# Performance work log

Measured on AMD Instinct MI355X. Metric: run time of the kernel, lower is better.

## Reference

```python
import jax, jax.numpy as jnp
import numpy as np
from jax import lax

D = 128      # d_model
NH = 8       # nhead
DIM = D // NH
B, H, W = 2, 160, 160
EPS_ATT = 1e-6


def setup_inputs() -> dict:
    key = jax.random.key(0)
    ks = iter(jax.random.split(key, 40))
    def n(*s):
        return jax.random.normal(next(ks), s, dtype=jnp.float32) * 0.05
    inp = {
        "x": jax.random.normal(next(ks), (B, D, H, W), jnp.float32),
        "source": jax.random.normal(next(ks), (B, D, H, W), jnp.float32),
        # q/k/v 1x1 conv (with bias)
        "wq": n(D, D), "bq": n(D),
        "wk": n(D, D), "bk": n(D),
        "wv": n(D, D), "bv": n(D),
        # multiscale aggregation (scale=5): depthwise 5x5 (no bias) + pointwise 1x1 (no bias)
        "dwq": n(D, 1, 5, 5), "pwq": n(D, D),
        "dwk": n(D, 1, 5, 5), "pwk": n(D, D),
        "dwv": n(D, 1, 5, 5), "pwv": n(D, D),
        # attention output projection: 2*d_model -> d_model, no bias
        "wproj": n(D, 2 * D),
        # merge 1x1 conv
        "wmerge": n(D, D), "bmerge": n(D),
        # conv ffn: d -> 2d -> d
        "wff1": n(2 * D, D), "bff1": n(2 * D),
        "wff2": n(D, 2 * D), "bff2": n(D),
        # layernorms over channel dim
        "ln1_w": 1.0 + n(D), "ln1_b": n(D),
        "ln2_w": 1.0 + n(D), "ln2_b": n(D),
    }
    return inp


def _pw(t, Wm, b=None):
    # 1x1 conv as channel matmul; t: [B,C,H,W], Wm: [O,C]
    y = jnp.einsum('bchw,oc->bohw', t, Wm)
    return y if b is None else y + b[None, :, None, None]


def _bn(t):
    # BatchNorm2d, training-mode batch stats, affine=False, eps=1e-5
    m = t.mean((0, 2, 3), keepdims=True)
    v = t.var((0, 2, 3), keepdims=True)
    return (t - m) * lax.rsqrt(v + 1e-5)


def _gelu(t):
    return jax.nn.gelu(t, approximate=False)


def _dw(t, Wk):
    # depthwise 5x5 conv, stride 1, SAME padding (== padding=2)
    return lax.conv_general_dilated(t, Wk, (1, 1), 'SAME',
                                    dimension_numbers=('NCHW', 'OIHW', 'NCHW'),
                                    feature_group_count=D)


def _ln(t, w, b):
    # LayerNorm over channel axis of NCHW tensor, eps=1e-5
    m = t.mean(1, keepdims=True)
    v = t.var(1, keepdims=True)
    return (t - m) * lax.rsqrt(v + 1e-5) * w[None, :, None, None] + b[None, :, None, None]


def reference(x, source, wq, bq, wk, bk, wv, bv, dwq, pwq, dwk, pwk, dwv, pwv,
              wproj, wmerge, bmerge, wff1, bff1, wff2, bff2,
              ln1_w, ln1_b, ln2_w, ln2_b):
    q = _gelu(_bn(_pw(x, wq, bq)))
    k = _gelu(_bn(_pw(source, wk, bk)))
    v = _gelu(_bn(_pw(source, wv, bv)))

    # multiscale aggregation: concat original with one scale-5 depthwise+pointwise branch
    qc = jnp.concatenate([q, _pw(_dw(q, dwq), pwq)], axis=1)
    kc = jnp.concatenate([k, _pw(_dw(k, dwk), pwk)], axis=1)
    vc = jnp.concatenate([v, _pw(_dw(v, dwv), pwv)], axis=1)

    qc = jax.nn.relu(qc)  # kernel feature map
    kc = jax.nn.relu(kc)

    b_, C2, h1, w1 = qc.shape           # C2 = 2*d_model
    h2, w2 = kc.shape[2], kc.shape[3]
    L1, L2 = h1 * w1, h2 * w2
    H2 = C2 // DIM                       # effective heads = 2*nhead

    qf = qc.reshape(b_, C2, L1).transpose(0, 2, 1).reshape(b_, L1, H2, DIM)
    kf = kc.reshape(b_, C2, L2).transpose(0, 2, 1).reshape(b_, L2, H2, DIM)
    vf = vc.reshape(b_, C2, L2).transpose(0, 2, 1).reshape(b_, L2, H2, DIM)

    vf = vf / L2
    kv = jnp.einsum('nshd,nshv->nhdv', kf, vf)                       # [b,H2,d,d]
    z = 1.0 / jnp.maximum(jnp.einsum('nlhd,nhd->nlh', qf, kf.sum(1) / L2), EPS_ATT)
    qv = jnp.einsum('nlhd,nhdv,nlh->nlhv', qf, kv, z)                # [b,L1,H2,d]

    out = qv.transpose(0, 2, 3, 1).reshape(b_, C2, h1, w1)
    msg = _pw(out, wproj)                                            # 2d -> d

    msg = _gelu(_bn(_pw(msg, wmerge, bmerge)))
    msg = x + msg
    msg = _ln(msg, ln1_w, ln1_b)

    ff = _gelu(_bn(_pw(msg, wff1, bff1)))
    ff = _gelu(_bn(_pw(ff, wff2, bff2)))
    return _ln(ff + msg, ln2_w, ln2_b)
```

## Files before the change

### kernel.cpp

```cpp
#include <hip/hip_runtime.h>
#include <math.h>

#define LL 25600
#define NTOTF 51200.f
#define NSH 8

using f16   = _Float16;
using f16x8 = __attribute__((ext_vector_type(8))) _Float16;
using f16x4 = __attribute__((ext_vector_type(4))) _Float16;
using f16x2 = __attribute__((ext_vector_type(2))) _Float16;
using f32x4 = __attribute__((ext_vector_type(4))) float;

__device__ __forceinline__ float gelu_f(float v) {
    const float u2 = v * (1.5957691216057308f + 0.0713548162726009f * v * v);
    const float e  = __expf(u2);
    return v * (1.f - 1.f / (e + 1.f));
}

__device__ __forceinline__ void stat_mr(const float* st, int C, int c,
                                        float& m, float& r) {
    float s1 = 0.f, s2 = 0.f;
#pragma unroll
    for (int sh = 0; sh < NSH; ++sh) {
        s1 += st[sh * 2 * C + c];
        s2 += st[sh * 2 * C + C + c];
    }
    m = s1 * (1.f / NTOTF);
    r = rsqrtf(s2 * (1.f / NTOTF) - m * m + 1e-5f);
}

template <int M, int K, int PP, int NSEG, bool IN32, bool LDG, bool TWOW,
          bool BIAS, bool STATS>
__global__ __launch_bounds__(512, 2) void gemm_kernel(
    const void* __restrict__ X1, const void* __restrict__ X2,
    const void* __restrict__ X3,
    const float* __restrict__ WA, const float* __restrict__ WB,
    const float* __restrict__ W2, const float* __restrict__ W3,
    const float* __restrict__ biasA, const float* __restrict__ biasB,
    const float* __restrict__ lstat,
    f16* __restrict__ Y1, f16* __restrict__ Y2, f16* __restrict__ Y3,
    float* __restrict__ ostat)
{
    constexpr int MR  = M / 128;
    constexpr int KS  = K / 32;
    constexpr int NR  = PP / 16;
    constexpr int PG  = PP / 8;
    constexpr int NCH = (K * PG) / 512;
    constexpr int NCHUNK = LL / PP;

    __shared__ f16 Xs[PP * K];

    const int tid  = threadIdx.x;
    const int lane = tid & 63;
    const int wv   = tid >> 6;
    const int lm16 = lane & 15, lg = lane >> 4;
    const int row0 = wv * (M / 8);

    int bx = blockIdx.x, seg = 0;
    if (NSEG > 1) { seg = bx / (2 * NCHUNK); bx -= seg * 2 * NCHUNK; }
    const int bb  = bx / NCHUNK;
    const int pp0 = (bx - bb * NCHUNK) * PP;

    const void*  Xp = (NSEG > 1) ? (seg == 0 ? X1 : (seg == 1 ? X2 : X3)) : X1;
    const float* Wp = (NSEG > 1) ? (seg == 0 ? WA : (seg == 1 ? W2 : W3)) : WA;
    f16*         Yp = (NSEG > 1) ? (seg == 0 ? Y1 : (seg == 1 ? Y2 : Y3)) : Y1;

    const int c0  = (tid / PG) * NCH;
    const int p0g = (tid % PG) * 8;

    f16x8 xin[NCH];
#pragma unroll
    for (int cc = 0; cc < NCH; ++cc) {
        const size_t roff = (size_t)(bb * K + c0 + cc) * LL + pp0 + p0g;
        if (IN32) {
            const float4 a  = *reinterpret_cast<const float4*>(
                                  reinterpret_cast<const float*>(Xp) + roff);
            const float4 b2 = *reinterpret_cast<const float4*>(
                                  reinterpret_cast<const float*>(Xp) + roff + 4);
            f16x8 v;
            v[0] = (f16)a.x;  v[1] = (f16)a.y;  v[2] = (f16)a.z;  v[3] = (f16)a.w;
            v[4] = (f16)b2.x; v[5] = (f16)b2.y; v[6] = (f16)b2.z; v[7] = (f16)b2.w;
            xin[cc] = v;
        } else {
            xin[cc] = *reinterpret_cast<const f16x8*>(
                          reinterpret_cast<const f16*>(Xp) + roff);
        }
    }

    f16x8 wfr[KS][MR];
#pragma unroll
    for (int k = 0; k < KS; ++k) {
        const int col = k * 32 + lg * 8;
#pragma unroll
        for (int mr = 0; mr < MR; ++mr) {
            const int row = row0 + mr * 16 + lm16;
            const float* wp = (TWOW && row >= 128)
                                  ? WB + (size_t)(row - 128) * K + col
                                  : Wp + (size_t)row * K + col;
            const float4 wa = *reinterpret_cast<const float4*>(wp);
            const float4 wb2 = *reinterpret_cast<const float4*>(wp + 4);
            f16x8 v;
            v[0] = (f16)wa.x; v[1] = (f16)wa.y; v[2] = (f16)wa.z; v[3] = (f16)wa.w;
            v[4] = (f16)wb2.x; v[5] = (f16)wb2.y; v[6] = (f16)wb2.z; v[7] = (f16)wb2.w;
            wfr[k][mr] = v;
        }
    }

    float bvv[MR], st1[MR], st2[MR];
#pragma unroll
    for (int mr = 0; mr < MR; ++mr) {
        const int o = row0 + mr * 16 + lm16;
        bvv[mr] = BIAS ? ((TWOW && o >= 128) ? biasB[o - 128] : biasA[o]) : 0.f;
        st1[mr] = 0.f; st2[mr] = 0.f;
    }

    if (LDG) {
#pragma unroll
        for (int cc = 0; cc < NCH; ++cc) {
            const int c = c0 + cc;
            float m, r;
            stat_mr(lstat, K, c, m, r);
#pragma unroll
            for (int j = 0; j < 8; ++j)
                xin[cc][j] = (f16)gelu_f(((float)xin[cc][j] - m) * r);
        }
    }

#pragma unroll
    for (int j = 0; j < 8; ++j) {
        const int pos = p0g + j;
        const int swz = ((pos & 7) ^ ((pos >> 3) & 7)) << 3;
        if constexpr (NCH == 8) {
            f16x8 v;
#pragma unroll
            for (int cc = 0; cc < 8; ++cc) v[cc] = xin[cc][j];
            *reinterpret_cast<f16x8*>(&Xs[(size_t)pos * K + (c0 ^ swz)]) = v;
        } else if constexpr (NCH == 4) {
            f16x4 v;
#pragma unroll
            for (int cc = 0; cc < 4; ++cc) v[cc] = xin[cc][j];
            *reinterpret_cast<f16x4*>(&Xs[(size_t)pos * K + (c0 ^ swz)]) = v;
        } else {
            f16x2 v;
#pragma unroll
            for (int cc = 0; cc < 2; ++cc) v[cc] = xin[cc][j];
            *reinterpret_cast<f16x2*>(&Xs[(size_t)pos * K + (c0 ^ swz)]) = v;
        }
    }
    __syncthreads();

    f32x4 acc[MR][NR];
#pragma unroll
    for (int mr = 0; mr < MR; ++mr)
#pragma unroll
        for (int nr = 0; nr < NR; ++nr)
            acc[mr][nr] = (f32x4){0.f, 0.f, 0.f, 0.f};

#pragma unroll
    for (int k = 0; k < KS; ++k) {
        const int kc = k * 32 + lg * 8;
        f16x8 xa[NR];
#pragma unroll
        for (int nr = 0; nr < NR; ++nr) {
            const int pos = nr * 16 + lm16;
            const int swz = ((pos & 7) ^ ((pos >> 3) & 7)) << 3;
            xa[nr] = *reinterpret_cast<const f16x8*>(
                &Xs[(size_t)pos * K + (kc ^ swz)]);
        }
#pragma unroll
        for (int mr = 0; mr < MR; ++mr)
#pragma unroll
            for (int nr = 0; nr < NR; ++nr)
                acc[mr][nr] = __builtin_amdgcn_mfma_f32_16x16x32_f16(
                    xa[nr], wfr[k][mr], acc[mr][nr], 0, 0, 0);
    }

#pragma unroll
    for (int mr = 0; mr < MR; ++mr) {
        const int o = row0 + mr * 16 + lm16;
        f16* yb = Yp + (size_t)(bb * M + o) * LL + pp0;
#pragma unroll
        for (int nr = 0; nr < NR; ++nr) {
            f16x4 o4;
#pragma unroll
            for (int r = 0; r < 4; ++r) {
                const float v = acc[mr][nr][r] + bvv[mr];
                o4[r] = (f16)v;
                if (STATS) { st1[mr] += v; st2[mr] += v * v; }
            }
            *reinterpret_cast<f16x4*>(yb + nr * 16 + lg * 4) = o4;
        }
    }

    if (STATS) {
        float* osb = ostat + (size_t)(blockIdx.x & (NSH - 1)) * 2 * M;
#pragma unroll
        for (int mr = 0; mr < MR; ++mr) {
            float s1 = st1[mr], s2 = st2[mr];
            s1 += __shfl_xor(s1, 16); s2 += __shfl_xor(s2, 16);
            s1 += __shfl_xor(s1, 32); s2 += __shfl_xor(s2, 32);
            if (lane < 16) {
                const int o = row0 + mr * 16 + lm16;
                atomicAdd(&osb[o], s1);
                atomicAdd(&osb[M + o], s2);
            }
        }
    }
}

__global__ __launch_bounds__(256) void act_kernel(
    const f16* __restrict__ qraw, const f16* __restrict__ kvraw,
    const float* __restrict__ sQ, const float* __restrict__ sKV,
    f16* __restrict__ actq, f16* __restrict__ actkv)
{
    const int idx = blockIdx.x * 256 + threadIdx.x;
    const f16* src; f16* dst; const float* st; int C, local;
    if (idx < 819200) { src = qraw;  dst = actq;  st = sQ;  C = 128; local = idx; }
    else              { src = kvraw; dst = actkv; st = sKV; C = 256; local = idx - 819200; }
    const int c = (local / 3200) % C;
    float m, r;
    stat_mr(st, C, c, m, r);
    const f16x8 v = *reinterpret_cast<const f16x8*>(src + (size_t)local * 8);
    f16x8 o;
#pragma unroll
    for (int j = 0; j < 8; ++j)
        o[j] = (f16)gelu_f(((float)v[j] - m) * r);
    *reinterpret_cast<f16x8*>(dst + (size_t)local * 8) = o;
}

__global__ __launch_bounds__(256) void dw5_kernel(
    const f16* __restrict__ actq, const f16* __restrict__ actkv,
    const float* __restrict__ dwq, const float* __restrict__ dwk,
    const float* __restrict__ dwv,
    f16* __restrict__ oq, f16* __restrict__ ok, f16* __restrict__ ov)
{
    __shared__ f16x2 pt[20][41];
    const int z = blockIdx.z;
    const int which = z >> 8;
    const int bc = z & 255;
    const int b = bc >> 7, c = bc & 127;

    const f16* src; const float* wdwp; f16* outp;
    if (which == 0)      { src = actq  + (size_t)(b * 128 + c) * LL;       wdwp = dwq + c * 25; outp = oq; }
    else if (which == 1) { src = actkv + (size_t)(b * 256 + c) * LL;       wdwp = dwk + c * 25; outp = ok; }
    else                 { src = actkv + (size_t)(b * 256 + 128 + c) * LL; wdwp = dwv + c * 25; outp = ov; }

    const int h0 = blockIdx.y * 32, w0 = blockIdx.x * 32;
    const int tid = threadIdx.x;

    f16x2 wp[25];
#pragma unroll
    for (int q = 0; q < 25; ++q) {
        const f16 wv16 = (f16)wdwp[q];
        wp[q][0] = wv16; wp[q][1] = wv16;
    }

    for (int idx = tid; idx < 720; idx += 256) {
        const int t  = idx / 36, cc = idx - t * 36;
        const int iw = w0 - 2 + cc;
        const int ih0 = h0 - 2 + t, ih1 = ih0 + 16;
        const int iwc  = min(max(iw, 0), 159);
        const int ihc0 = min(max(ih0, 0), 159);
        const int ihc1 = min(max(ih1, 0), 159);
        const bool okw = (iw >= 0) & (iw < 160);
        f16 lo = src[ihc0 * 160 + iwc];
        f16 hi = src[ihc1 * 160 + iwc];
        if (!(okw & (ih0 >= 0) & (ih0 < 160))) lo = (f16)0;
        if (!(okw & (ih1 >= 0) & (ih1 < 160))) hi = (f16)0;
        f16x2 pv; pv[0] = lo; pv[1] = hi;
        pt[t][cc] = pv;
    }
    __syncthreads();

    const int ylo = tid >> 4, xq = tid & 15, x0 = xq * 2;

    f16x2 a0; a0[0] = (f16)0; a0[1] = (f16)0;
    f16x2 a1 = a0;
#pragma unroll
    for (int u = 0; u < 5; ++u) {
        const f16x2* row = &pt[ylo + u][x0];
        const f16x2 r0 = row[0], r1 = row[1], r2 = row[2];
        const f16x2 r3 = row[3], r4 = row[4], r5 = row[5];
        a0 += wp[u*5+0] * r0;  a1 += wp[u*5+0] * r1;
        a0 += wp[u*5+1] * r1;  a1 += wp[u*5+1] * r2;
        a0 += wp[u*5+2] * r2;  a1 += wp[u*5+2] * r3;
        a0 += wp[u*5+3] * r3;  a1 += wp[u*5+3] * r4;
        a0 += wp[u*5+4] * r4;  a1 += wp[u*5+4] * r5;
    }

    f16* ob = outp + (size_t)(b * 128 + c) * LL + (size_t)(h0 + ylo) * 160 + (w0 + x0);
    f16x2 lo2; lo2[0] = a0[0]; lo2[1] = a1[0];
    f16x2 hi2; hi2[0] = a0[1]; hi2[1] = a1[1];
    *reinterpret_cast<f16x2*>(ob) = lo2;
    *reinterpret_cast<f16x2*>(ob + 16 * 160) = hi2;
}

__global__ __launch_bounds__(256) void att_reduce_kernel(
    const f16* __restrict__ ACT, const f16* __restrict__ K2,
    const f16* __restrict__ V2,
    float* __restrict__ kvout, float* __restrict__ ksum)
{
    __shared__ float kvred[4][256];

    const int bx = blockIdx.x;
    const int b = bx / 400;
    const int rem = bx - b * 400;
    const int h = rem / 25;
    const int chunk = rem - h * 25;
    const int tid = threadIdx.x;
    const int wv = tid >> 6, l = tid & 63;
    const int ch = l & 15, kg = l >> 4;
    const bool half1 = h < 8;

    const f16* kbase = half1 ? ACT + (size_t)(b * 256 + h * 16 + ch) * LL
                             : K2 + (size_t)(b * 128 + (h - 8) * 16 + ch) * LL;
    const f16* vbase = half1 ? ACT + (size_t)(b * 256 + 128 + h * 16 + ch) * LL
                             : V2 + (size_t)(b * 128 + (h - 8) * 16 + ch) * LL;

    f32x4 acc = (f32x4){0.f, 0.f, 0.f, 0.f};
    float ksacc = 0.f;
    const int base = chunk * 1024 + kg * 8;
#pragma unroll
    for (int it = 0; it < 8; ++it) {
        const int p = base + wv * 256 + it * 32;
        const f16x8 kf = *reinterpret_cast<const f16x8*>(kbase + p);
        const f16x8 vf = *reinterpret_cast<const f16x8*>(vbase + p);
        f16x8 ka;
#pragma unroll
        for (int j = 0; j < 8; ++j) {
            const f16 kv_ = kf[j];
            ka[j] = (kv_ > (f16)0) ? kv_ : (f16)0;
            ksacc += (float)ka[j];
        }
        acc = __builtin_amdgcn_mfma_f32_16x16x32_f16(ka, vf, acc, 0, 0, 0);
    }

    constexpr float s = 1.f / (float)LL;
#pragma unroll
    for (int r = 0; r < 4; ++r)
        kvred[wv][(kg * 4 + r) * 16 + ch] = acc[r];
    __syncthreads();
    {
        float t = kvred[0][tid] + kvred[1][tid] + kvred[2][tid] + kvred[3][tid];
        atomicAdd(&kvout[(size_t)(b * 16 + h) * 256 + tid], t * s);
    }

    float s1 = ksacc;
    s1 += __shfl_xor(s1, 16);
    s1 += __shfl_xor(s1, 32);
    if (l < 16) atomicAdd(&ksum[(size_t)(b * 16 + h) * 16 + ch], s1 * s);
}

__global__ __launch_bounds__(256) void att_apply_kernel(
    const f16* __restrict__ Q, const f16* __restrict__ Q2,
    const float* __restrict__ kvin, const float* __restrict__ ksumin,
    f16* __restrict__ att)
{
    __shared__ float kvs[256];
    __shared__ float kss[16];

    const int bx = blockIdx.x;
    const int b = bx / 1600;
    const int rem = bx - b * 1600;
    const int h = rem / 100;
    const int chunk = rem - h * 100;
    const int tid = threadIdx.x;
    const int p = chunk * 256 + tid;

    kvs[tid] = kvin[(size_t)b * 4096 + h * 256 + tid];
    if (tid < 16) kss[tid] = ksumin[(size_t)b * 256 + h * 16 + tid];
    __syncthreads();

    const f16* qb = (h < 8) ? Q + (size_t)(b * 128 + h * 16) * LL
                            : Q2 + (size_t)(b * 128 + (h - 8) * 16) * LL;
    float s[16];
#pragma unroll
    for (int d = 0; d < 16; ++d)
        s[d] = fmaxf((float)qb[(size_t)d * LL + p], 0.f);
    float denom = 0.f;
#pragma unroll
    for (int d = 0; d < 16; ++d) denom = fmaf(s[d], kss[d], denom);
    const float z = 1.f / fmaxf(denom, 1e-6f);

    f16* ob = att + (size_t)(b * 256 + h * 16) * LL + p;
#pragma unroll
    for (int e = 0; e < 16; ++e) {
        float acc = 0.f;
#pragma unroll
        for (int d = 0; d < 16; ++d)
            acc = fmaf(s[d], kvs[d * 16 + e], acc);
        ob[(size_t)e * LL] = (f16)(acc * z);
    }
}

template <bool RES32, bool OUT32>
__global__ __launch_bounds__(256) void fuse_ln_kernel(
    const f16* __restrict__ yconv, const void* __restrict__ residv,
    const float* __restrict__ stat,
    const float* __restrict__ lnw, const float* __restrict__ lnb,
    void* __restrict__ outv)
{
    __shared__ float t[128][64];
    __shared__ float mrs[128][2];
    __shared__ float red[4][64][2];
    __shared__ float mln[64], rln[64];

    const int bx = blockIdx.x;
    const int b = bx / 400, p0 = (bx - b * 400) * 64;
    const int tid = threadIdx.x;

    if (tid < 128) {
        float m, r;
        stat_mr(stat, 128, tid, m, r);
        mrs[tid][0] = m; mrs[tid][1] = r;
    }
    __syncthreads();

    for (int idx = tid; idx < 8192; idx += 256) {
        const int c = idx >> 6, i = idx & 63;
        const size_t off = (size_t)(b * 128 + c) * LL + p0 + i;
        const float g = gelu_f(((float)yconv[off] - mrs[c][0]) * mrs[c][1]);
        const float r = RES32 ? reinterpret_cast<const float*>(residv)[off]
                              : (float)reinterpret_cast<const f16*>(residv)[off];
        t[c][i] = g + r;
    }
    __syncthreads();

    {
        const int i = tid & 63, q = tid >> 6;
        float ps = 0.f, pq = 0.f;
        for (int c = q * 32; c < q * 32 + 32; ++c) {
            const float v = t[c][i];
            ps += v; pq += v * v;
        }
        red[q][i][0] = ps; red[q][i][1] = pq;
    }
    __syncthreads();
    if (tid < 64) {
        float s1 = 0.f, s2 = 0.f;
#pragma unroll
        for (int q = 0; q < 4; ++q) { s1 += red[q][tid][0]; s2 += red[q][tid][1]; }
        const float m = s1 * (1.f / 128.f);
        const float var = s2 * (1.f / 128.f) - m * m;
        mln[tid] = m; rln[tid] = rsqrtf(var + 1e-5f);
    }
    __syncthreads();

    for (int idx = tid; idx < 8192; idx += 256) {
        const int c = idx >> 6, i = idx & 63;
        const float v = (t[c][i] - mln[i]) * rln[i] * lnw[c] + lnb[c];
        const size_t off = (size_t)(b * 128 + c) * LL + p0 + i;
        if (OUT32) reinterpret_cast<float*>(outv)[off] = v;
        else reinterpret_cast<f16*>(outv)[off] = (f16)v;
    }
}

__global__ __launch_bounds__(256) void wcomb_kernel(
    const float* __restrict__ wmerge, const float* __restrict__ wproj,
    float* __restrict__ wc)
{
    const int o = blockIdx.x;
    const int c2 = threadIdx.x;
    float acc = 0.f;
#pragma unroll 4
    for (int m = 0; m < 128; ++m)
        acc = fmaf(wmerge[o * 128 + m], wproj[m * 256 + c2], acc);
    wc[o * 256 + c2] = acc;
}

extern "C" void kernel_launch(void* const* d_in, const int* in_sizes, int n_in,
                              void* d_out, int out_size, void* d_ws, size_t ws_size,
                              hipStream_t stream)
{
    const float* x      = (const float*)d_in[0];
    const float* source = (const float*)d_in[1];
    const float* wq = (const float*)d_in[2];  const float* bq = (const float*)d_in[3];
    const float* wk = (const float*)d_in[4];  const float* bk = (const float*)d_in[5];
    const float* wvw = (const float*)d_in[6]; const float* bvb = (const float*)d_in[7];
    const float* dwq = (const float*)d_in[8];  const float* pwq = (const float*)d_in[9];
    const float* dwk = (const float*)d_in[10]; const float* pwk = (const float*)d_in[11];
    const float* dwv = (const float*)d_in[12]; const float* pwv = (const float*)d_in[13];
    const float* wproj  = (const float*)d_in[14];
    const float* wmerge = (const float*)d_in[15]; const float* bmerge = (const float*)d_in[16];
    const float* wff1 = (const float*)d_in[17]; const float* bff1 = (const float*)d_in[18];
    const float* wff2 = (const float*)d_in[19]; const float* bff2 = (const float*)d_in[20];
    const float* ln1w = (const float*)d_in[21]; const float* ln1b = (const float*)d_in[22];
    const float* ln2w = (const float*)d_in[23]; const float* ln2b = (const float*)d_in[24];

    const size_t UNIT  = (size_t)2 * 128 * LL;
    const size_t UNITB = UNIT * sizeof(f16);
    char* w = (char*)d_ws;
    f16* qraw  = (f16*)w; w += UNITB;
    f16* kvraw = (f16*)w; w += 2 * UNITB;
    f16* actq  = (f16*)w; w += UNITB;
    f16* actkv = (f16*)w; w += 2 * UNITB;
    f16* q2raw = (f16*)w; w += UNITB;
    f16* k2raw = (f16*)w; w += UNITB;
    f16* v2raw = (f16*)w; w += UNITB;
    f16* y2raw = (f16*)w; w += UNITB;
    f16* msg   = (f16*)w; w += UNITB;
    f16* ff1raw= (f16*)w; w += 2 * UNITB;
    f16* ff2raw= (f16*)w; w += UNITB;

    f16* dtq = qraw;
    f16* dtk = kvraw;
    f16* dtv = kvraw + UNIT;
    f16* att = actkv;

    float* zbase = (float*)w;
    float* kvred = zbase;
    float* ksum  = zbase + 8192;
    float* sQ    = zbase + 8704;
    float* sKV   = sQ + NSH * 256;
    float* sM    = sKV + NSH * 512;
    float* sF1   = sM + NSH * 256;
    float* sF2   = sF1 + NSH * 512;
    const size_t zcount = 8192 + 512 + NSH * (256 + 512 + 256 + 512 + 256);
    float* wcomb = zbase + zcount;

    hipMemsetAsync(zbase, 0, zcount * sizeof(float), stream);
    wcomb_kernel<<<128, 256, 0, stream>>>(wmerge, wproj, wcomb);

    gemm_kernel<128,128,128,1,true,false,false,true,true><<<400, 512, 0, stream>>>(
        x, nullptr, nullptr, wq, nullptr, nullptr, nullptr, bq, nullptr, nullptr,
        qraw, nullptr, nullptr, sQ);
    gemm_kernel<256,128,64,1,true,false,true,true,true><<<800, 512, 0, stream>>>(
        source, nullptr, nullptr, wk, wvw, nullptr, nullptr, bk, bvb, nullptr,
        kvraw, nullptr, nullptr, sKV);

    act_kernel<<<9600, 256, 0, stream>>>(qraw, kvraw, sQ, sKV, actq, actkv);

    dim3 dwg(5, 5, 768);
    dw5_kernel<<<dwg, 256, 0, stream>>>(actq, actkv, dwq, dwk, dwv, dtq, dtk, dtv);
    gemm_kernel<128,128,128,3,false,false,false,false,false><<<1200, 512, 0, stream>>>(
        dtq, dtk, dtv, pwq, nullptr, pwk, pwv, nullptr, nullptr, nullptr,
        q2raw, k2raw, v2raw, nullptr);

    att_reduce_kernel<<<800, 256, 0, stream>>>(actkv, k2raw, v2raw, kvred, ksum);
    att_apply_kernel<<<3200, 256, 0, stream>>>(actq, q2raw, kvred, ksum, att);

    gemm_kernel<128,256,128,1,false,false,false,true,true><<<400, 512, 0, stream>>>(
        att, nullptr, nullptr, wcomb, nullptr, nullptr, nullptr, bmerge, nullptr,
        nullptr, y2raw, nullptr, nullptr, sM);

    fuse_ln_kernel<true,false><<<800, 256, 0, stream>>>(
        y2raw, x, sM, ln1w, ln1b, msg);

    gemm_kernel<256,128,64,1,false,false,false,true,true><<<800, 512, 0, stream>>>(
        msg, nullptr, nullptr, wff1, nullptr, nullptr, nullptr, bff1, nullptr,
        nullptr, ff1raw, nullptr, nullptr, sF1);
    gemm_kernel<128,256,128,1,false,true,false,true,true><<<400, 512, 0, stream>>>(
        ff1raw, nullptr, nullptr, wff2, nullptr, nullptr, nullptr, bff2, nullptr,
        sF1, ff2raw, nullptr, nullptr, sF2);

    fuse_ln_kernel<false,true><<<800, 256, 0, stream>>>(
        ff2raw, msg, sF2, ln2w, ln2b, (float*)d_out);
}
```

Before: 273.3 us.

## Fuse attention apply with merged projection GEMM into one kernel

Replaces the separate attention-apply kernel and the following 256->128 projection GEMM with a single kernel. Each block computes the linear-attention output for 64 pixels across all 16 heads into swizzled shared memory, then runs MFMA against the combined weight and accumulates BN statistics. This removes the write and re-read of the 256-channel fp16 attention tensor and one launch. In exchange, each block redundantly loads all kv matrices and converts weights, and it uses more shared memory per block.

```diff
diff --git a/kernel.cpp b/kernel.cpp
--- a/kernel.cpp
+++ b/kernel.cpp
@@ -208,6 +208,127 @@
     }
 }
 
+__global__ __launch_bounds__(512, 2) void att_merge_kernel(
+    const f16* __restrict__ Q, const f16* __restrict__ Q2,
+    const float* __restrict__ kvin, const float* __restrict__ ksumin,
+    const float* __restrict__ wc, const float* __restrict__ bias,
+    f16* __restrict__ Y, float* __restrict__ ostat)
+{
+    __shared__ f16 Xs[64 * 256];
+    __shared__ float kvs[4096];
+    __shared__ float kss[256];
+
+    const int tid  = threadIdx.x;
+    const int lane = tid & 63;
+    const int wv   = tid >> 6;
+    const int lm16 = lane & 15, lg = lane >> 4;
+    const int row0 = wv * 16;
+
+    const int bx = blockIdx.x;
+    const int b  = bx / 400;
+    const int p0 = (bx - b * 400) * 64;
+
+    for (int i = tid; i < 4096; i += 512) kvs[i] = kvin[(size_t)b * 4096 + i];
+    if (tid < 256) kss[tid] = ksumin[b * 256 + tid];
+
+    f16x8 wfr[8];
+#pragma unroll
+    for (int k = 0; k < 8; ++k) {
+        const int col = k * 32 + lg * 8;
+        const float* wp = wc + (size_t)(row0 + lm16) * 256 + col;
+        const float4 wa = *reinterpret_cast<const float4*>(wp);
+        const float4 wb2 = *reinterpret_cast<const float4*>(wp + 4);
+        f16x8 v;
+        v[0] = (f16)wa.x; v[1] = (f16)wa.y; v[2] = (f16)wa.z; v[3] = (f16)wa.w;
+        v[4] = (f16)wb2.x; v[5] = (f16)wb2.y; v[6] = (f16)wb2.z; v[7] = (f16)wb2.w;
+        wfr[k] = v;
+    }
+    const float bvv = bias[row0 + lm16];
+    float st1 = 0.f, st2 = 0.f;
+
+    __syncthreads();
+
+    const int pl = tid & 63;
+    const int p  = p0 + pl;
+    const int hg = tid >> 6;
+    const int swzp = ((pl & 7) ^ ((pl >> 3) & 7)) << 3;
+#pragma unroll
+    for (int it = 0; it < 2; ++it) {
+        const int h = hg * 2 + it;
+        const f16* qb = (h < 8) ? Q + (size_t)(b * 128 + h * 16) * LL
+                                : Q2 + (size_t)(b * 128 + (h - 8) * 16) * LL;
+        float s[16];
+#pragma unroll
+        for (int d = 0; d < 16; ++d)
+            s[d] = fmaxf((float)qb[(size_t)d * LL + p], 0.f);
+        float denom = 0.f;
+#pragma unroll
+        for (int d = 0; d < 16; ++d) denom = fmaf(s[d], kss[h * 16 + d], denom);
+        const float z = 1.f / fmaxf(denom, 1e-6f);
+
+        f16x8 v0, v1;
+#pragma unroll
+        for (int e = 0; e < 8; ++e) {
+            float a0 = 0.f, a1 = 0.f;
+#pragma unroll
+            for (int d = 0; d < 16; ++d) {
+                a0 = fmaf(s[d], kvs[h * 256 + d * 16 + e], a0);
+                a1 = fmaf(s[d], kvs[h * 256 + d * 16 + 8 + e], a1);
+            }
+            v0[e] = (f16)(a0 * z);
+            v1[e] = (f16)(a1 * z);
+        }
+        *reinterpret_cast<f16x8*>(&Xs[(size_t)pl * 256 + ((h * 16) ^ swzp)]) = v0;
+        *reinterpret_cast<f16x8*>(&Xs[(size_t)pl * 256 + ((h * 16 + 8) ^ swzp)]) = v1;
+    }
+    __syncthreads();
+
+    f32x4 acc[4];
+#pragma unroll
+    for (int nr = 0; nr < 4; ++nr) acc[nr] = (f32x4){0.f, 0.f, 0.f, 0.f};
+
+#pragma unroll
+    for (int k = 0; k < 8; ++k) {
+        const int kc = k * 32 + lg * 8;
+        f16x8 xa[4];
+#pragma unroll
+        for (int nr = 0; nr < 4; ++nr) {
+            const int pos = nr * 16 + lm16;
+            const int swz = ((pos & 7) ^ ((pos >> 3) & 7)) << 3;
+            xa[nr] = *reinterpret_cast<const f16x8*>(
+                &Xs[(size_t)pos * 256 + (kc ^ swz)]);
+        }
+#pragma unroll
+        for (int nr = 0; nr < 4; ++nr)
+            acc[nr] = __builtin_amdgcn_mfma_f32_16x16x32_f16(
+                xa[nr], wfr[k], acc[nr], 0, 0, 0);
+    }
+
+    {
+        const int o = row0 + lm16;
+        f16* yb = Y + (size_t)(b * 128 + o) * LL + p0;
+#pragma unroll
+        for (int nr = 0; nr < 4; ++nr) {
+            f16x4 o4;
+#pragma unroll
+            for (int r = 0; r < 4; ++r) {
+                const float v = acc[nr][r] + bvv;
+                o4[r] = (f16)v;
+                st1 += v; st2 += v * v;
+            }
+            *reinterpret_cast<f16x4*>(yb + nr * 16 + lg * 4) = o4;
+        }
+        float* osb = ostat + (size_t)(blockIdx.x & (NSH - 1)) * 256;
+        float s1 = st1, s2 = st2;
+        s1 += __shfl_xor(s1, 16); s2 += __shfl_xor(s2, 16);
+        s1 += __shfl_xor(s1, 32); s2 += __shfl_xor(s2, 32);
+        if (lane < 16) {
+            atomicAdd(&osb[o], s1);
+            atomicAdd(&osb[128 + o], s2);
+        }
+    }
+}
+
 __global__ __launch_bounds__(256) void act_kernel(
     const f16* __restrict__ qraw, const f16* __restrict__ kvraw,
     const float* __restrict__ sQ, const float* __restrict__ sKV,
@@ -351,48 +472,6 @@
     if (l < 16) atomicAdd(&ksum[(size_t)(b * 16 + h) * 16 + ch], s1 * s);
 }
 
-__global__ __launch_bounds__(256) void att_apply_kernel(
-    const f16* __restrict__ Q, const f16* __restrict__ Q2,
-    const float* __restrict__ kvin, const float* __restrict__ ksumin,
-    f16* __restrict__ att)
-{
-    __shared__ float kvs[256];
-    __shared__ float kss[16];
-
-    const int bx = blockIdx.x;
-    const int b = bx / 1600;
-    const int rem = bx - b * 1600;
-    const int h = rem / 100;
-    const int chunk = rem - h * 100;
-    const int tid = threadIdx.x;
-    const int p = chunk * 256 + tid;
-
-    kvs[tid] = kvin[(size_t)b * 4096 + h * 256 + tid];
-    if (tid < 16) kss[tid] = ksumin[(size_t)b * 256 + h * 16 + tid];
-    __syncthreads();
-
-    const f16* qb = (h < 8) ? Q + (size_t)(b * 128 + h * 16) * LL
-                            : Q2 + (size_t)(b * 128 + (h - 8) * 16) * LL;
-    float s[16];
-#pragma unroll
-    for (int d = 0; d < 16; ++d)
-        s[d] = fmaxf((float)qb[(size_t)d * LL + p], 0.f);
-    float denom = 0.f;
-#pragma unroll
-    for (int d = 0; d < 16; ++d) denom = fmaf(s[d], kss[d], denom);
-    const float z = 1.f / fmaxf(denom, 1e-6f);
-
-    f16* ob = att + (size_t)(b * 256 + h * 16) * LL + p;
-#pragma unroll
-    for (int e = 0; e < 16; ++e) {
-        float acc = 0.f;
-#pragma unroll
-        for (int d = 0; d < 16; ++d)
-            acc = fmaf(s[d], kvs[d * 16 + e], acc);
-        ob[(size_t)e * LL] = (f16)(acc * z);
-    }
-}
-
 template <bool RES32, bool OUT32>
 __global__ __launch_bounds__(256) void fuse_ln_kernel(
     const f16* __restrict__ yconv, const void* __restrict__ residv,
@@ -505,7 +584,6 @@
     f16* dtq = qraw;
     f16* dtk = kvraw;
     f16* dtv = kvraw + UNIT;
-    f16* att = actkv;
 
     float* zbase = (float*)w;
     float* kvred = zbase;
@@ -537,11 +615,8 @@
         q2raw, k2raw, v2raw, nullptr);
 
     att_reduce_kernel<<<800, 256, 0, stream>>>(actkv, k2raw, v2raw, kvred, ksum);
-    att_apply_kernel<<<3200, 256, 0, stream>>>(actq, q2raw, kvred, ksum, att);
-
-    gemm_kernel<128,256,128,1,false,false,false,true,true><<<400, 512, 0, stream>>>(
-        att, nullptr, nullptr, wcomb, nullptr, nullptr, nullptr, bmerge, nullptr,
-        nullptr, y2raw, nullptr, nullptr, sM);
+    att_merge_kernel<<<800, 512, 0, stream>>>(actq, q2raw, kvred, ksum,
+                                              wcomb, bmerge, y2raw, sM);
 
     fuse_ln_kernel<true,false><<<800, 256, 0, stream>>>(
         y2raw, x, sM, ln1w, ln1b, msg);
```

Result: slower. 293.2 us (+7.3%).
